# Kernel tuning notes

Measured on AMD Instinct MI355X. Metric: run time of the kernel, lower is better.

The kernel has to match this reference:

```python
import jax, jax.numpy as jnp
import numpy as np

DIM = 128
WS = 7          # window size
NH = 4          # num heads
N = WS * WS     # tokens per window = 49
GRID = 56       # 224/4 token grid -> 8x8 = 64 windows per image
NUM_WIN = (GRID // WS) ** 2  # 64
IMG_B = 64
SCALE = (DIM // NH) ** -0.5


def _relative_position_index():
    coords = np.stack(np.meshgrid(np.arange(WS), np.arange(WS), indexing='ij'))  # (2,WS,WS)
    flat = coords.reshape(2, -1)                         # (2, N)
    rel = flat[:, :, None] - flat[:, None, :]            # (2, N, N)
    rel = rel.transpose(1, 2, 0).astype(np.int32)        # (N, N, 2)
    rel[:, :, 0] += WS - 1
    rel[:, :, 1] += WS - 1
    rel[:, :, 0] *= 2 * WS - 1
    return jnp.asarray(rel.sum(-1))                      # (N, N) int32


def _shift_mask():
    # Swin shifted-window attention mask: shift = WS // 2, off-group pairs get -100.
    shift = WS // 2
    img = np.zeros((GRID, GRID), dtype=np.int32)
    cnt = 0
    segs = (slice(0, -WS), slice(-WS, -shift), slice(-shift, None))
    for hs in segs:
        for ws_ in segs:
            img[hs, ws_] = cnt
            cnt += 1
    # window partition -> (NUM_WIN, N)
    w = img.reshape(GRID // WS, WS, GRID // WS, WS).transpose(0, 2, 1, 3).reshape(NUM_WIN, N)
    diff = w[:, :, None] - w[:, None, :]
    return jnp.asarray(np.where(diff != 0, -100.0, 0.0).astype(np.float32))  # (NUM_WIN, N, N)


def setup_inputs() -> dict:
    key = jax.random.key(0)
    ks = jax.random.split(key, 6)
    B = IMG_B * NUM_WIN  # 4096
    x = jax.random.normal(ks[0], (B, N, DIM), dtype=jnp.float32)
    qkv_w = jax.random.normal(ks[1], (3 * DIM, DIM), dtype=jnp.float32) * (DIM ** -0.5)
    qkv_b = jnp.zeros((3 * DIM,), dtype=jnp.float32)
    proj_w = jax.random.normal(ks[2], (DIM, DIM), dtype=jnp.float32) * (DIM ** -0.5)
    proj_b = jnp.zeros((DIM,), dtype=jnp.float32)
    rel_bias_table = jax.random.normal(ks[3], ((2 * WS - 1) ** 2, NH), dtype=jnp.float32) * 0.02
    return {
        'x': x,
        'mask': _shift_mask(),
        'qkv_w': qkv_w,
        'qkv_b': qkv_b,
        'proj_w': proj_w,
        'proj_b': proj_b,
        'rel_bias_table': rel_bias_table,
        'rel_index': _relative_position_index(),
    }


def reference(x, mask, qkv_w, qkv_b, proj_w, proj_b, rel_bias_table, rel_index):
    B, n, C = x.shape
    hd = C // NH
    qkv = (x @ qkv_w.T + qkv_b).reshape(B, n, 3, NH, hd)
    q = qkv[:, :, 0].transpose(0, 2, 1, 3) * SCALE   # (B, H, N, hd)
    k = qkv[:, :, 1].transpose(0, 2, 1, 3)
    v = qkv[:, :, 2].transpose(0, 2, 1, 3)
    attn = jnp.einsum('bhnd,bhmd->bhnm', q, k)       # (B, H, N, N)
    bias = rel_bias_table[rel_index.reshape(-1)].reshape(n, n, NH).transpose(2, 0, 1)
    attn = attn + bias[None]
    nW = mask.shape[0]
    attn = attn.reshape(B // nW, nW, NH, n, n) + mask[None, :, None]
    attn = jax.nn.softmax(attn.reshape(B, NH, n, n), axis=-1)
    out = jnp.einsum('bhnm,bhmd->bhnd', attn, v).transpose(0, 2, 1, 3).reshape(B, n, C)
    return out @ proj_w.T + proj_b
```

## Files before the change

### kernel.cpp

```cpp
#include <hip/hip_runtime.h>


#define NTOK  49
#define DIMC  128
#define NBLK  4096
#define SCALE 0.17677669529663687f
#define LOG2E 1.4426950408889634f
#define NMASK -144.26950408889634f

typedef __attribute__((ext_vector_type(8))) short bf16x8;
typedef __attribute__((ext_vector_type(4))) float f32x4;

#define WS_QKVW 0
#define WS_PROJW 49152
#define WS_BIAS  65536

#define QPO_OFF 0
#define KX_OFF  6272
#define VB_OFF  12544
#define VB_STRIDE 56
#define SMEM_TOT 19720

#define SWZ(r, c) ((r) * 128 + ((c) ^ (((r) & 7) << 3)))

__device__ __forceinline__ unsigned int pkbf2(float f0, float f1) {
    union { float f; unsigned int i; } a, b; a.f = f0; b.f = f1;
    return __builtin_amdgcn_perm(b.i + 0x8000u, a.i + 0x8000u, 0x07060302u);
}
__device__ __forceinline__ unsigned short f2b_r(float f) {
    union { float f; unsigned int i; } v; v.f = f;
    return (unsigned short)((v.i + 0x8000u) >> 16);
}
__device__ __forceinline__ float b2f_lo(unsigned int u) {
    union { unsigned int i; float f; } v; v.i = u << 16; return v.f;
}
__device__ __forceinline__ float b2f_hi(unsigned int u) {
    union { unsigned int i; float f; } v; v.i = u & 0xFFFF0000u; return v.f;
}
__device__ __forceinline__ float exp2_hw(float x) {
    float r; asm("v_exp_f32 %0, %1" : "=v"(r) : "v"(x)); return r;
}

__device__ __forceinline__ int seg3(int c) { return (c < 49) ? 0 : ((c < 53) ? 1 : 2); }

__global__ __launch_bounds__(256)
void prep(const float* __restrict__ qkv_w, const float* __restrict__ proj_w,
          const float* __restrict__ bias_t, const int* __restrict__ rel_idx,
          unsigned short* __restrict__ ws)
{
    int idx = blockIdx.x * 256 + threadIdx.x;
    if (idx < 8192) {
        int base = idx * 8;
        const float* sp = (base < 49152) ? (qkv_w + base) : (proj_w + (base - 49152));
        float sc = (base < 16384) ? (SCALE * LOG2E) : 1.0f;
        float4 a = *(const float4*)sp;
        float4 b = *(const float4*)(sp + 4);
        uint4 u;
        u.x = pkbf2(a.x * sc, a.y * sc);
        u.y = pkbf2(a.z * sc, a.w * sc);
        u.z = pkbf2(b.x * sc, b.y * sc);
        u.w = pkbf2(b.z * sc, b.w * sc);
        *(uint4*)(ws + base) = u;
    } else {
        int i = idx - 8192;
        int reg = i & 3, lane = (i >> 2) & 63, nt = (i >> 8) & 3,
            mt = (i >> 10) & 3, h = (i >> 12) & 3;
        int row = mt * 16 + (lane >> 4) * 4 + reg;
        int col = nt * 16 + (lane & 15);
        float v = 0.f;
        if (row < NTOK && col < NTOK)
            v = bias_t[rel_idx[row * NTOK + col] * 4 + h] * LOG2E;
        ws[WS_BIAS + i] = f2b_r(v);
    }
}

__global__ __launch_bounds__(512, 4)
void win_attn(const float* __restrict__ x,
              const float* __restrict__ qkv_b,
              const float* __restrict__ proj_b,
              const unsigned short* __restrict__ ws,
              float* __restrict__ out)
{
    __shared__ unsigned short smem[SMEM_TOT];
    const int b    = blockIdx.x;
    const int w    = b & 63;
    const int tid  = threadIdx.x;
    const int wv   = tid >> 6;
    const int lane = tid & 63;
    const int qg   = lane >> 4;
    const int l15  = lane & 15;

    if (tid == 0) {
        uint4 z = { 0u, 0u, 0u, 0u };
        *(uint4*)(smem + VB_OFF + 127 * VB_STRIDE + VB_STRIDE) = z;
    }

    {
        const float4* xg = (const float4*)(x + (size_t)b * (NTOK * DIMC));
        #pragma unroll
        for (int it = 0; it < 4; it++) {
            int i = tid + it * 512;
            if (i < NTOK * DIMC / 4) {
                float4 v = xg[i];
                int row = i >> 5, col = (i & 31) * 4;
                uint2 u; u.x = pkbf2(v.x, v.y); u.y = pkbf2(v.z, v.w);
                *(uint2*)(smem + KX_OFF + SWZ(row, col)) = u;
            }
        }
    }
    __syncthreads();

    uint2 kreg[4];
    {
        const unsigned short* qw = ws + WS_QKVW;
        const int h2 = wv >> 1;
        const int dhalf = wv & 1;
        const int dh = dhalf * 16 + l15;
        float bias_pp[3];
        #pragma unroll
        for (int pp = 0; pp < 3; pp++) {
            int j = (pp * 8 + wv) * 16 + l15;
            bias_pp[pp] = (pp == 0) ? qkv_b[j] * (SCALE * LOG2E) : qkv_b[j];
        }
        #pragma unroll
        for (int mt = 0; mt < 4; mt++) {
            int ar = mt * 16 + l15; if (ar > 48) ar = 48;
            bf16x8 af[4];
            #pragma unroll
            for (int ks_ = 0; ks_ < 4; ks_++)
                af[ks_] = *(const bf16x8*)(smem + KX_OFF + SWZ(ar, ks_ * 32 + qg * 8));
            #pragma unroll
            for (int pp = 0; pp < 3; pp++) {
                const int j = (pp * 8 + wv) * 16 + l15;
                f32x4 acc = { bias_pp[pp], bias_pp[pp], bias_pp[pp], bias_pp[pp] };
                #pragma unroll
                for (int ks_ = 0; ks_ < 4; ks_++) {
                    bf16x8 bfr = *(const bf16x8*)(qw + j * DIMC + ks_ * 32 + qg * 8);
                    acc = __builtin_amdgcn_mfma_f32_16x16x32_bf16(af[ks_], bfr, acc, 0, 0, 0);
                }
                if (pp == 0) {
                    #pragma unroll
                    for (int r = 0; r < 4; r++) {
                        int row = mt * 16 + qg * 4 + r;
                        if (row < NTOK)
                            smem[QPO_OFF + SWZ(row, h2 * 32 + dh)] = f2b_r(acc[r]);
                    }
                } else if (pp == 1) {
                    kreg[mt].x = pkbf2(acc[0], acc[1]);
                    kreg[mt].y = pkbf2(acc[2], acc[3]);
                } else {
                    int tokbase = mt * 16 + qg * 4;
                    if (tokbase <= 52) {
                        uint2 u; u.x = pkbf2(acc[0], acc[1]); u.y = pkbf2(acc[2], acc[3]);
                        *(uint2*)(smem + VB_OFF + (h2 * 32 + dh) * VB_STRIDE + tokbase) = u;
                    }
                }
            }
        }
    }
    __syncthreads();
    {
        const int h2 = wv >> 1;
        const int dh = (wv & 1) * 16 + l15;
        #pragma unroll
        for (int mt = 0; mt < 4; mt++) {
            unsigned short kv0 = (unsigned short)(kreg[mt].x & 0xFFFFu);
            unsigned short kv1 = (unsigned short)(kreg[mt].x >> 16);
            unsigned short kv2 = (unsigned short)(kreg[mt].y & 0xFFFFu);
            unsigned short kv3 = (unsigned short)(kreg[mt].y >> 16);
            int row = mt * 16 + qg * 4;
            if (row     < NTOK) smem[KX_OFF + SWZ(row,     h2 * 32 + dh)] = kv0;
            if (row + 1 < NTOK) smem[KX_OFF + SWZ(row + 1, h2 * 32 + dh)] = kv1;
            if (row + 2 < NTOK) smem[KX_OFF + SWZ(row + 2, h2 * 32 + dh)] = kv2;
            if (row + 3 < NTOK) smem[KX_OFF + SWZ(row + 3, h2 * 32 + dh)] = kv3;
        }
    }
    __syncthreads();

    const int g  = wv >> 2;
    const int st = wv & 3;
    const int r0 = st * 16;
    const int wy = w >> 3, wx = w & 7;
    int grow[4];
    #pragma unroll
    for (int r = 0; r < 4; r++) {
        int t = r0 + qg * 4 + r;
        int ty = (t * 9363) >> 16, tx = t - ty * 7;
        grow[r] = seg3(wy * 7 + ty) * 3 + seg3(wx * 7 + tx);
    }
    int arq = r0 + l15; if (arq > 48) arq = 48;

    const bf16x8 aq0 = *(const bf16x8*)(smem + QPO_OFF + SWZ(arq, (2 * g) * 32 + qg * 8));
    const bf16x8 aq1 = *(const bf16x8*)(smem + QPO_OFF + SWZ(arq, (2 * g + 1) * 32 + qg * 8));

    #pragma unroll
    for (int hh = 0; hh < 2; hh++) {
        const int h = 2 * g + hh;
        const bf16x8 aq = hh ? aq1 : aq0;
        float sv[4][4];
        #pragma unroll
        for (int nt = 0; nt < 4; nt++) {
            int krow = nt * 16 + l15; if (krow > 48) krow = 48;
            bf16x8 bk = *(const bf16x8*)(smem + KX_OFF + SWZ(krow, h * 32 + qg * 8));
            f32x4 z = { 0.f, 0.f, 0.f, 0.f };
            f32x4 c = __builtin_amdgcn_mfma_f32_16x16x32_bf16(aq, bk, z, 0, 0, 0);
            uint2 bb = *(const uint2*)(ws + WS_BIAS + (((h * 4 + st) * 4 + nt) * 64 + lane) * 4);
            int t = nt * 16 + l15;
            int ty = (t * 9363) >> 16, tx = t - ty * 7;
            int gcol = seg3(wy * 7 + ty) * 3 + seg3(wx * 7 + tx);
            bool vc = t < NTOK;
            float bv[4] = { b2f_lo(bb.x), b2f_hi(bb.x), b2f_lo(bb.y), b2f_hi(bb.y) };
            #pragma unroll
            for (int r = 0; r < 4; r++) {
                float v = c[r] + bv[r] + ((grow[r] == gcol) ? 0.f : NMASK);
                sv[nt][r] = vc ? v : -1e30f;
            }
        }
        float inv[4];
        #pragma unroll
        for (int r = 0; r < 4; r++) {
            float mx = fmaxf(fmaxf(sv[0][r], sv[1][r]), fmaxf(sv[2][r], sv[3][r]));
            mx = fmaxf(mx, __shfl_xor(mx, 1));
            mx = fmaxf(mx, __shfl_xor(mx, 2));
            mx = fmaxf(mx, __shfl_xor(mx, 4));
            mx = fmaxf(mx, __shfl_xor(mx, 8));
            float sum = 0.f;
            #pragma unroll
            for (int nt = 0; nt < 4; nt++) {
                float e = exp2_hw(sv[nt][r] - mx);
                sv[nt][r] = e; sum += e;
            }
            sum += __shfl_xor(sum, 1);
            sum += __shfl_xor(sum, 2);
            sum += __shfl_xor(sum, 4);
            sum += __shfl_xor(sum, 8);
            inv[r] = __builtin_amdgcn_rcpf(sum);
        }
        #pragma unroll
        for (int nt = 0; nt < 4; nt++)
            #pragma unroll
            for (int r = 0; r < 4; r++) {
                int row = r0 + qg * 4 + r;
                if (row < NTOK)
                    smem[QPO_OFF + SWZ(row, g * 64 + nt * 16 + l15)] = f2b_r(sv[nt][r]);
            }
        f32x4 accO[2] = { { 0.f, 0.f, 0.f, 0.f }, { 0.f, 0.f, 0.f, 0.f } };
        #pragma unroll
        for (int ks2 = 0; ks2 < 2; ks2++) {
            bf16x8 ap = *(const bf16x8*)(smem + QPO_OFF + SWZ(arq, g * 64 + ks2 * 32 + qg * 8));
            #pragma unroll
            for (int nt2 = 0; nt2 < 2; nt2++) {
                bf16x8 bvv = *(const bf16x8*)(smem + VB_OFF
                              + (h * 32 + nt2 * 16 + l15) * VB_STRIDE + ks2 * 32 + qg * 8);
                accO[nt2] = __builtin_amdgcn_mfma_f32_16x16x32_bf16(ap, bvv, accO[nt2], 0, 0, 0);
            }
        }
        if (hh == 0) {
            __syncthreads();
            #pragma unroll
            for (int nt2 = 0; nt2 < 2; nt2++)
                #pragma unroll
                for (int r = 0; r < 4; r++) {
                    int row = r0 + qg * 4 + r;
                    if (row < NTOK)
                        smem[KX_OFF + SWZ(row, g * 64 + nt2 * 16 + l15)] =
                            f2b_r(accO[nt2][r] * inv[r]);
                }
        } else {
            #pragma unroll
            for (int nt2 = 0; nt2 < 2; nt2++)
                #pragma unroll
                for (int r = 0; r < 4; r++) {
                    int row = r0 + qg * 4 + r;
                    if (row < NTOK)
                        smem[QPO_OFF + SWZ(row, g * 64 + nt2 * 16 + l15)] =
                            f2b_r(accO[nt2][r] * inv[r]);
                }
        }
    }
    __syncthreads();

    {
        const int mt = wv & 3, jh = wv >> 2;
        int ar = mt * 16 + l15; if (ar > 48) ar = 48;
        bf16x8 ad[4];
        #pragma unroll
        for (int ks_ = 0; ks_ < 4; ks_++) {
            int base = (ks_ >> 1) * 64 + qg * 8;
            ad[ks_] = (ks_ & 1)
                ? *(const bf16x8*)(smem + QPO_OFF + SWZ(ar, base))
                : *(const bf16x8*)(smem + KX_OFF  + SWZ(ar, base));
        }
        const unsigned short* pw = ws + WS_PROJW;
        float* ob = out + (size_t)b * (NTOK * DIMC);
        #pragma unroll
        for (int jt2 = 0; jt2 < 4; jt2++) {
            const int j = jh * 64 + jt2 * 16 + l15;
            bf16x8 bfr[4];
            #pragma unroll
            for (int ks_ = 0; ks_ < 4; ks_++)
                bfr[ks_] = *(const bf16x8*)(pw + j * DIMC + ks_ * 32 + qg * 8);
            const float pb = proj_b[j];
            f32x4 acc = { pb, pb, pb, pb };
            #pragma unroll
            for (int ks_ = 0; ks_ < 4; ks_++)
                acc = __builtin_amdgcn_mfma_f32_16x16x32_bf16(ad[ks_], bfr[ks_], acc, 0, 0, 0);
            #pragma unroll
            for (int r = 0; r < 4; r++) {
                int row = mt * 16 + qg * 4 + r;
                if (row < NTOK) ob[row * DIMC + j] = acc[r];
            }
        }
    }
}

extern "C" void kernel_launch(void* const* d_in, const int* in_sizes, int n_in,
                              void* d_out, int out_size, void* d_ws, size_t ws_size,
                              hipStream_t stream) {
    const float* x      = (const float*)d_in[0];
    const float* qkv_w  = (const float*)d_in[2];
    const float* qkv_b  = (const float*)d_in[3];
    const float* proj_w = (const float*)d_in[4];
    const float* proj_b = (const float*)d_in[5];
    const float* bias_t = (const float*)d_in[6];
    const int*   relidx = (const int*)d_in[7];
    float*       outp   = (float*)d_out;
    unsigned short* ws  = (unsigned short*)d_ws;

    prep<<<96, 256, 0, stream>>>(qkv_w, proj_w, bias_t, relidx, ws);
    win_attn<<<NBLK, 512, 0, stream>>>(x, qkv_b, proj_b, ws, outp);
}
```

Before: 308.2 us.

## Make window-attention kernel persistent with double-buffered LDS across eight windows

Each block now processes eight consecutive windows instead of one, using two LDS context buffers so the next window's x staging overlaps attention and the previous window's projection overlaps the next QKV phase. The attention output for both heads is kept in registers and written once to the Q buffer, which removes one intra-attention barrier and the split KX/QPO layout for the projection input. The aim is to hide global load latency and cut per-block launch and sync overhead. In exchange the grid shrinks to 512 blocks, which may underfill the GPU, and LDS use per block doubles, which lowers occupancy.

Result: slower. 557.2 us (+80.8%).

```diff
diff --git a/kernel.cpp b/kernel.cpp
--- a/kernel.cpp
+++ b/kernel.cpp
@@ -3,7 +3,8 @@
 
 #define NTOK  49
 #define DIMC  128
-#define NBLK  4096
+#define NW    8
+#define NBLK2 512
 #define SCALE 0.17677669529663687f
 #define LOG2E 1.4426950408889634f
 #define NMASK -144.26950408889634f
@@ -19,7 +20,7 @@
 #define KX_OFF  6272
 #define VB_OFF  12544
 #define VB_STRIDE 56
-#define SMEM_TOT 19720
+#define CTX     19720
 
 #define SWZ(r, c) ((r) * 128 + ((c) ^ (((r) & 7) << 3)))
 
@@ -40,7 +41,6 @@
 __device__ __forceinline__ float exp2_hw(float x) {
     float r; asm("v_exp_f32 %0, %1" : "=v"(r) : "v"(x)); return r;
 }
-
 __device__ __forceinline__ int seg3(int c) { return (c < 49) ? 0 : ((c < 53) ? 1 : 2); }
 
 __global__ __launch_bounds__(256)
@@ -74,109 +74,92 @@
     }
 }
 
-__global__ __launch_bounds__(512, 4)
-void win_attn(const float* __restrict__ x,
-              const float* __restrict__ qkv_b,
-              const float* __restrict__ proj_b,
-              const unsigned short* __restrict__ ws,
-              float* __restrict__ out)
-{
-    __shared__ unsigned short smem[SMEM_TOT];
-    const int b    = blockIdx.x;
-    const int w    = b & 63;
-    const int tid  = threadIdx.x;
-    const int wv   = tid >> 6;
-    const int lane = tid & 63;
-    const int qg   = lane >> 4;
-    const int l15  = lane & 15;
-
-    if (tid == 0) {
-        uint4 z = { 0u, 0u, 0u, 0u };
-        *(uint4*)(smem + VB_OFF + 127 * VB_STRIDE + VB_STRIDE) = z;
-    }
-
-    {
-        const float4* xg = (const float4*)(x + (size_t)b * (NTOK * DIMC));
-        #pragma unroll
-        for (int it = 0; it < 4; it++) {
-            int i = tid + it * 512;
-            if (i < NTOK * DIMC / 4) {
-                float4 v = xg[i];
-                int row = i >> 5, col = (i & 31) * 4;
-                uint2 u; u.x = pkbf2(v.x, v.y); u.y = pkbf2(v.z, v.w);
-                *(uint2*)(smem + KX_OFF + SWZ(row, col)) = u;
-            }
-        }
-    }
-    __syncthreads();
-
-    uint2 kreg[4];
-    {
-        const unsigned short* qw = ws + WS_QKVW;
-        const int h2 = wv >> 1;
-        const int dhalf = wv & 1;
-        const int dh = dhalf * 16 + l15;
-        float bias_pp[3];
+__device__ __forceinline__ void stage_x(unsigned short* sm, const float* xb, int tid)
+{
+    const float4* xg = (const float4*)xb;
+    #pragma unroll
+    for (int it = 0; it < 4; it++) {
+        int i = tid + it * 512;
+        if (i < NTOK * DIMC / 4) {
+            float4 v = xg[i];
+            int row = i >> 5, col = (i & 31) * 4;
+            uint2 u; u.x = pkbf2(v.x, v.y); u.y = pkbf2(v.z, v.w);
+            *(uint2*)(sm + KX_OFF + SWZ(row, col)) = u;
+        }
+    }
+}
+
+__device__ __forceinline__ void qkv_phase(unsigned short* sm, const unsigned short* qw,
+        const float* qkv_b, int wv, int qg, int l15, uint2 kreg[4])
+{
+    const int h2 = wv >> 1;
+    const int dhalf = wv & 1;
+    const int dh = dhalf * 16 + l15;
+    float bias_pp[3];
+    #pragma unroll
+    for (int pp = 0; pp < 3; pp++) {
+        int j = (pp * 8 + wv) * 16 + l15;
+        bias_pp[pp] = (pp == 0) ? qkv_b[j] * (SCALE * LOG2E) : qkv_b[j];
+    }
+    #pragma unroll
+    for (int mt = 0; mt < 4; mt++) {
+        int ar = mt * 16 + l15; if (ar > 48) ar = 48;
+        bf16x8 af[4];
+        #pragma unroll
+        for (int ks_ = 0; ks_ < 4; ks_++)
+            af[ks_] = *(const bf16x8*)(sm + KX_OFF + SWZ(ar, ks_ * 32 + qg * 8));
         #pragma unroll
         for (int pp = 0; pp < 3; pp++) {
-            int j = (pp * 8 + wv) * 16 + l15;
-            bias_pp[pp] = (pp == 0) ? qkv_b[j] * (SCALE * LOG2E) : qkv_b[j];
-        }
-        #pragma unroll
-        for (int mt = 0; mt < 4; mt++) {
-            int ar = mt * 16 + l15; if (ar > 48) ar = 48;
-            bf16x8 af[4];
-            #pragma unroll
-            for (int ks_ = 0; ks_ < 4; ks_++)
-                af[ks_] = *(const bf16x8*)(smem + KX_OFF + SWZ(ar, ks_ * 32 + qg * 8));
-            #pragma unroll
-            for (int pp = 0; pp < 3; pp++) {
-                const int j = (pp * 8 + wv) * 16 + l15;
-                f32x4 acc = { bias_pp[pp], bias_pp[pp], bias_pp[pp], bias_pp[pp] };
+            const int j = (pp * 8 + wv) * 16 + l15;
+            f32x4 acc = { bias_pp[pp], bias_pp[pp], bias_pp[pp], bias_pp[pp] };
+            #pragma unroll
+            for (int ks_ = 0; ks_ < 4; ks_++) {
+                bf16x8 bfr = *(const bf16x8*)(qw + j * DIMC + ks_ * 32 + qg * 8);
+                acc = __builtin_amdgcn_mfma_f32_16x16x32_bf16(af[ks_], bfr, acc, 0, 0, 0);
+            }
+            if (pp == 0) {
                 #pragma unroll
-                for (int ks_ = 0; ks_ < 4; ks_++) {
-                    bf16x8 bfr = *(const bf16x8*)(qw + j * DIMC + ks_ * 32 + qg * 8);
-                    acc = __builtin_amdgcn_mfma_f32_16x16x32_bf16(af[ks_], bfr, acc, 0, 0, 0);
+                for (int r = 0; r < 4; r++) {
+                    int row = mt * 16 + qg * 4 + r;
+                    if (row < NTOK)
+                        sm[QPO_OFF + SWZ(row, h2 * 32 + dh)] = f2b_r(acc[r]);
                 }
-                if (pp == 0) {
-                    #pragma unroll
-                    for (int r = 0; r < 4; r++) {
-                        int row = mt * 16 + qg * 4 + r;
-                        if (row < NTOK)
-                            smem[QPO_OFF + SWZ(row, h2 * 32 + dh)] = f2b_r(acc[r]);
-                    }
-                } else if (pp == 1) {
-                    kreg[mt].x = pkbf2(acc[0], acc[1]);
-                    kreg[mt].y = pkbf2(acc[2], acc[3]);
-                } else {
-                    int tokbase = mt * 16 + qg * 4;
-                    if (tokbase <= 52) {
-                        uint2 u; u.x = pkbf2(acc[0], acc[1]); u.y = pkbf2(acc[2], acc[3]);
-                        *(uint2*)(smem + VB_OFF + (h2 * 32 + dh) * VB_STRIDE + tokbase) = u;
-                    }
+            } else if (pp == 1) {
+                kreg[mt].x = pkbf2(acc[0], acc[1]);
+                kreg[mt].y = pkbf2(acc[2], acc[3]);
+            } else {
+                int tokbase = mt * 16 + qg * 4;
+                if (tokbase <= 52) {
+                    uint2 u; u.x = pkbf2(acc[0], acc[1]); u.y = pkbf2(acc[2], acc[3]);
+                    *(uint2*)(sm + VB_OFF + (h2 * 32 + dh) * VB_STRIDE + tokbase) = u;
                 }
             }
         }
     }
-    __syncthreads();
-    {
-        const int h2 = wv >> 1;
-        const int dh = (wv & 1) * 16 + l15;
-        #pragma unroll
-        for (int mt = 0; mt < 4; mt++) {
-            unsigned short kv0 = (unsigned short)(kreg[mt].x & 0xFFFFu);
-            unsigned short kv1 = (unsigned short)(kreg[mt].x >> 16);
-            unsigned short kv2 = (unsigned short)(kreg[mt].y & 0xFFFFu);
-            unsigned short kv3 = (unsigned short)(kreg[mt].y >> 16);
-            int row = mt * 16 + qg * 4;
-            if (row     < NTOK) smem[KX_OFF + SWZ(row,     h2 * 32 + dh)] = kv0;
-            if (row + 1 < NTOK) smem[KX_OFF + SWZ(row + 1, h2 * 32 + dh)] = kv1;
-            if (row + 2 < NTOK) smem[KX_OFF + SWZ(row + 2, h2 * 32 + dh)] = kv2;
-            if (row + 3 < NTOK) smem[KX_OFF + SWZ(row + 3, h2 * 32 + dh)] = kv3;
-        }
-    }
-    __syncthreads();
-
+}
+
+__device__ __forceinline__ void k_writeback(unsigned short* sm, const uint2 kreg[4],
+        int wv, int qg, int l15)
+{
+    const int h2 = wv >> 1;
+    const int dh = (wv & 1) * 16 + l15;
+    #pragma unroll
+    for (int mt = 0; mt < 4; mt++) {
+        unsigned short kv0 = (unsigned short)(kreg[mt].x & 0xFFFFu);
+        unsigned short kv1 = (unsigned short)(kreg[mt].x >> 16);
+        unsigned short kv2 = (unsigned short)(kreg[mt].y & 0xFFFFu);
+        unsigned short kv3 = (unsigned short)(kreg[mt].y >> 16);
+        int row = mt * 16 + qg * 4;
+        if (row     < NTOK) sm[KX_OFF + SWZ(row,     h2 * 32 + dh)] = kv0;
+        if (row + 1 < NTOK) sm[KX_OFF + SWZ(row + 1, h2 * 32 + dh)] = kv1;
+        if (row + 2 < NTOK) sm[KX_OFF + SWZ(row + 2, h2 * 32 + dh)] = kv2;
+        if (row + 3 < NTOK) sm[KX_OFF + SWZ(row + 3, h2 * 32 + dh)] = kv3;
+    }
+}
+
+__device__ __forceinline__ void attn_phase(unsigned short* sm, const unsigned short* wsb,
+        int w, int wv, int lane, int qg, int l15)
+{
     const int g  = wv >> 2;
     const int st = wv & 3;
     const int r0 = st * 16;
@@ -190,8 +173,12 @@
     }
     int arq = r0 + l15; if (arq > 48) arq = 48;
 
-    const bf16x8 aq0 = *(const bf16x8*)(smem + QPO_OFF + SWZ(arq, (2 * g) * 32 + qg * 8));
-    const bf16x8 aq1 = *(const bf16x8*)(smem + QPO_OFF + SWZ(arq, (2 * g + 1) * 32 + qg * 8));
+    const bf16x8 aq0 = *(const bf16x8*)(sm + QPO_OFF + SWZ(arq, (2 * g) * 32 + qg * 8));
+    const bf16x8 aq1 = *(const bf16x8*)(sm + QPO_OFF + SWZ(arq, (2 * g + 1) * 32 + qg * 8));
+
+    f32x4 accO[2][2] = { { {0.f,0.f,0.f,0.f}, {0.f,0.f,0.f,0.f} },
+                         { {0.f,0.f,0.f,0.f}, {0.f,0.f,0.f,0.f} } };
+    float invv[2][4];
 
     #pragma unroll
     for (int hh = 0; hh < 2; hh++) {
@@ -201,10 +188,10 @@
         #pragma unroll
         for (int nt = 0; nt < 4; nt++) {
             int krow = nt * 16 + l15; if (krow > 48) krow = 48;
-            bf16x8 bk = *(const bf16x8*)(smem + KX_OFF + SWZ(krow, h * 32 + qg * 8));
+            bf16x8 bk = *(const bf16x8*)(sm + KX_OFF + SWZ(krow, h * 32 + qg * 8));
             f32x4 z = { 0.f, 0.f, 0.f, 0.f };
             f32x4 c = __builtin_amdgcn_mfma_f32_16x16x32_bf16(aq, bk, z, 0, 0, 0);
-            uint2 bb = *(const uint2*)(ws + WS_BIAS + (((h * 4 + st) * 4 + nt) * 64 + lane) * 4);
+            uint2 bb = *(const uint2*)(wsb + (((h * 4 + st) * 4 + nt) * 64 + lane) * 4);
             int t = nt * 16 + l15;
             int ty = (t * 9363) >> 16, tx = t - ty * 7;
             int gcol = seg3(wy * 7 + ty) * 3 + seg3(wx * 7 + tx);
@@ -216,7 +203,6 @@
                 sv[nt][r] = vc ? v : -1e30f;
             }
         }
-        float inv[4];
         #pragma unroll
         for (int r = 0; r < 4; r++) {
             float mx = fmaxf(fmaxf(sv[0][r], sv[1][r]), fmaxf(sv[2][r], sv[3][r]));
@@ -234,7 +220,7 @@
             sum += __shfl_xor(sum, 2);
             sum += __shfl_xor(sum, 4);
             sum += __shfl_xor(sum, 8);
-            inv[r] = __builtin_amdgcn_rcpf(sum);
+            invv[hh][r] = __builtin_amdgcn_rcpf(sum);
         }
         #pragma unroll
         for (int nt = 0; nt < 4; nt++)
@@ -242,76 +228,110 @@
             for (int r = 0; r < 4; r++) {
                 int row = r0 + qg * 4 + r;
                 if (row < NTOK)
-                    smem[QPO_OFF + SWZ(row, g * 64 + nt * 16 + l15)] = f2b_r(sv[nt][r]);
-            }
-        f32x4 accO[2] = { { 0.f, 0.f, 0.f, 0.f }, { 0.f, 0.f, 0.f, 0.f } };
+                    sm[QPO_OFF + SWZ(row, g * 64 + nt * 16 + l15)] = f2b_r(sv[nt][r]);
+            }
         #pragma unroll
         for (int ks2 = 0; ks2 < 2; ks2++) {
-            bf16x8 ap = *(const bf16x8*)(smem + QPO_OFF + SWZ(arq, g * 64 + ks2 * 32 + qg * 8));
+            bf16x8 ap = *(const bf16x8*)(sm + QPO_OFF + SWZ(arq, g * 64 + ks2 * 32 + qg * 8));
             #pragma unroll
             for (int nt2 = 0; nt2 < 2; nt2++) {
-                bf16x8 bvv = *(const bf16x8*)(smem + VB_OFF
+                bf16x8 bvv = *(const bf16x8*)(sm + VB_OFF
                               + (h * 32 + nt2 * 16 + l15) * VB_STRIDE + ks2 * 32 + qg * 8);
-                accO[nt2] = __builtin_amdgcn_mfma_f32_16x16x32_bf16(ap, bvv, accO[nt2], 0, 0, 0);
-            }
-        }
-        if (hh == 0) {
-            __syncthreads();
-            #pragma unroll
-            for (int nt2 = 0; nt2 < 2; nt2++)
-                #pragma unroll
-                for (int r = 0; r < 4; r++) {
-                    int row = r0 + qg * 4 + r;
-                    if (row < NTOK)
-                        smem[KX_OFF + SWZ(row, g * 64 + nt2 * 16 + l15)] =
-                            f2b_r(accO[nt2][r] * inv[r]);
-                }
-        } else {
-            #pragma unroll
-            for (int nt2 = 0; nt2 < 2; nt2++)
-                #pragma unroll
-                for (int r = 0; r < 4; r++) {
-                    int row = r0 + qg * 4 + r;
-                    if (row < NTOK)
-                        smem[QPO_OFF + SWZ(row, g * 64 + nt2 * 16 + l15)] =
-                            f2b_r(accO[nt2][r] * inv[r]);
-                }
-        }
-    }
+                accO[hh][nt2] = __builtin_amdgcn_mfma_f32_16x16x32_bf16(ap, bvv, accO[hh][nt2], 0, 0, 0);
+            }
+        }
+    }
+    #pragma unroll
+    for (int hh = 0; hh < 2; hh++)
+        #pragma unroll
+        for (int nt2 = 0; nt2 < 2; nt2++)
+            #pragma unroll
+            for (int r = 0; r < 4; r++) {
+                int row = r0 + qg * 4 + r;
+                if (row < NTOK)
+                    sm[QPO_OFF + SWZ(row, (2 * g + hh) * 32 + nt2 * 16 + l15)] =
+                        f2b_r(accO[hh][nt2][r] * invv[hh][r]);
+            }
+}
+
+__device__ __forceinline__ void proj_phase(const unsigned short* sm, const unsigned short* pw,
+        const float* proj_b, float* ob, int wv, int qg, int l15)
+{
+    const int mt = wv & 3, jh = wv >> 2;
+    int ar = mt * 16 + l15; if (ar > 48) ar = 48;
+    bf16x8 ad[4];
+    #pragma unroll
+    for (int ks_ = 0; ks_ < 4; ks_++)
+        ad[ks_] = *(const bf16x8*)(sm + QPO_OFF + SWZ(ar, ks_ * 32 + qg * 8));
+    #pragma unroll
+    for (int jt2 = 0; jt2 < 4; jt2++) {
+        const int j = jh * 64 + jt2 * 16 + l15;
+        bf16x8 bfr[4];
+        #pragma unroll
+        for (int ks_ = 0; ks_ < 4; ks_++)
+            bfr[ks_] = *(const bf16x8*)(pw + j * DIMC + ks_ * 32 + qg * 8);
+        const float pb = proj_b[j];
+        f32x4 acc = { pb, pb, pb, pb };
+        #pragma unroll
+        for (int ks_ = 0; ks_ < 4; ks_++)
+            acc = __builtin_amdgcn_mfma_f32_16x16x32_bf16(ad[ks_], bfr[ks_], acc, 0, 0, 0);
+        #pragma unroll
+        for (int r = 0; r < 4; r++) {
+            int row = mt * 16 + qg * 4 + r;
+            if (row < NTOK) ob[row * DIMC + j] = acc[r];
+        }
+    }
+}
+
+__global__ __launch_bounds__(512, 4)
+void win_attn(const float* __restrict__ x,
+              const float* __restrict__ qkv_b,
+              const float* __restrict__ proj_b,
+              const unsigned short* __restrict__ ws,
+              float* __restrict__ out)
+{
+    __shared__ unsigned short smem[2 * CTX];
+    const int tid  = threadIdx.x;
+    const int wv   = tid >> 6;
+    const int lane = tid & 63;
+    const int qg   = lane >> 4;
+    const int l15  = lane & 15;
+
+    if (tid == 0) {
+        uint4 z = { 0u, 0u, 0u, 0u };
+        *(uint4*)(smem + VB_OFF + 7168) = z;
+        *(uint4*)(smem + CTX + VB_OFF + 7168) = z;
+    }
+
+    const unsigned short* qw  = ws + WS_QKVW;
+    const unsigned short* pw  = ws + WS_PROJW;
+    const unsigned short* wsb = ws + WS_BIAS;
+    const int bbase = blockIdx.x * NW;
+
+    stage_x(smem, x + (size_t)bbase * (NTOK * DIMC), tid);
     __syncthreads();
 
-    {
-        const int mt = wv & 3, jh = wv >> 2;
-        int ar = mt * 16 + l15; if (ar > 48) ar = 48;
-        bf16x8 ad[4];
-        #pragma unroll
-        for (int ks_ = 0; ks_ < 4; ks_++) {
-            int base = (ks_ >> 1) * 64 + qg * 8;
-            ad[ks_] = (ks_ & 1)
-                ? *(const bf16x8*)(smem + QPO_OFF + SWZ(ar, base))
-                : *(const bf16x8*)(smem + KX_OFF  + SWZ(ar, base));
-        }
-        const unsigned short* pw = ws + WS_PROJW;
-        float* ob = out + (size_t)b * (NTOK * DIMC);
-        #pragma unroll
-        for (int jt2 = 0; jt2 < 4; jt2++) {
-            const int j = jh * 64 + jt2 * 16 + l15;
-            bf16x8 bfr[4];
-            #pragma unroll
-            for (int ks_ = 0; ks_ < 4; ks_++)
-                bfr[ks_] = *(const bf16x8*)(pw + j * DIMC + ks_ * 32 + qg * 8);
-            const float pb = proj_b[j];
-            f32x4 acc = { pb, pb, pb, pb };
-            #pragma unroll
-            for (int ks_ = 0; ks_ < 4; ks_++)
-                acc = __builtin_amdgcn_mfma_f32_16x16x32_bf16(ad[ks_], bfr[ks_], acc, 0, 0, 0);
-            #pragma unroll
-            for (int r = 0; r < 4; r++) {
-                int row = mt * 16 + qg * 4 + r;
-                if (row < NTOK) ob[row * DIMC + j] = acc[r];
-            }
-        }
-    }
+    uint2 kreg[4];
+    for (int i = 0; i < NW; ++i) {
+        unsigned short* sc = smem + (i & 1) * CTX;
+        unsigned short* so = smem + ((i & 1) ^ 1) * CTX;
+        const int bi = bbase + i;
+
+        qkv_phase(sc, qw, qkv_b, wv, qg, l15, kreg);
+        if (i > 0)
+            proj_phase(so, pw, proj_b, out + (size_t)(bi - 1) * (NTOK * DIMC), wv, qg, l15);
+        __syncthreads();
+
+        k_writeback(sc, kreg, wv, qg, l15);
+        __syncthreads();
+
+        attn_phase(sc, wsb, bi & 63, wv, lane, qg, l15);
+        if (i + 1 < NW)
+            stage_x(so, x + (size_t)(bi + 1) * (NTOK * DIMC), tid);
+        __syncthreads();
+    }
+    proj_phase(smem + ((NW - 1) & 1) * CTX, pw, proj_b,
+               out + (size_t)(bbase + NW - 1) * (NTOK * DIMC), wv, qg, l15);
 }
 
 extern "C" void kernel_launch(void* const* d_in, const int* in_sizes, int n_in,
@@ -328,5 +348,5 @@
     unsigned short* ws  = (unsigned short*)d_ws;
 
     prep<<<96, 256, 0, stream>>>(qkv_w, proj_w, bias_t, relidx, ws);
-    win_attn<<<NBLK, 512, 0, stream>>>(x, qkv_b, proj_b, ws, outp);
-}
+    win_attn<<<NBLK2, 512, 0, stream>>>(x, qkv_b, proj_b, ws, outp);
+}
```
